# Optimization experiments

Measured on AMD Instinct MI355X. Metric: run time of the kernel, lower is better.

The kernel has to match this reference:

```python
import jax, jax.numpy as jnp
import numpy as np

INV_SQRT2 = np.float32(1.0 / np.sqrt(2.0))


def _dwt1(x, axis):
    # pywt db1 (Haar), even-length: cA=(even+odd)/sqrt2, cD=(even-odd)/sqrt2
    ev = jax.lax.slice_in_dim(x, 0, None, 2, axis)
    od = jax.lax.slice_in_dim(x, 1, None, 2, axis)
    return (ev + od) * INV_SQRT2, (ev - od) * INV_SQRT2


def _idwt1(lo, hi, axis):
    ev = (lo + hi) * INV_SQRT2
    od = (lo - hi) * INV_SQRT2
    st = jnp.stack([ev, od], axis=axis + 1)  # (.., n, 2, ..)
    new_shape = list(lo.shape)
    new_shape[axis] *= 2
    return st.reshape(new_shape)


def haar_dwt2(x):
    lo, hi = _dwt1(x, 1)      # along width
    ll, lh = _dwt1(lo, 0)     # along height
    hl, hh = _dwt1(hi, 0)
    return ll, lh, hl, hh


def haar_idwt2(ll, lh, hl, hh):
    lo = _idwt1(ll, lh, 0)
    hi = _idwt1(hl, hh, 0)
    return _idwt1(lo, hi, 1)


def conv_same(img, w, b):
    # img: [h, w] -> 1x1-channel SAME conv with bias
    y = jax.lax.conv_general_dilated(
        img[None, None], w, (1, 1), 'SAME',
        dimension_numbers=('NCHW', 'OIHW', 'NCHW'))
    return y[0, 0] + b[0]


def setup_inputs() -> dict:
    key = jax.random.key(0)
    ks = jax.random.split(key, 7)
    H = W = 4096
    return {
        'x': jax.random.normal(ks[0], (1, 1, H, W), dtype=jnp.float32),
        'w3': jax.random.normal(ks[1], (1, 1, 3, 3), dtype=jnp.float32) * 0.1,
        'b3': jax.random.normal(ks[2], (1,), dtype=jnp.float32) * 0.1,
        'w5': jax.random.normal(ks[3], (1, 1, 5, 5), dtype=jnp.float32) * 0.1,
        'b5': jax.random.normal(ks[4], (1,), dtype=jnp.float32) * 0.1,
        'w7': jax.random.normal(ks[5], (1, 1, 7, 7), dtype=jnp.float32) * 0.1,
        'b7': jax.random.normal(ks[6], (1,), dtype=jnp.float32) * 0.1,
    }


def reference(x, w3, b3, w5, b5, w7, b7):
    img = x[0, 0]
    # 3-level wavedec2: collect details finest -> coarsest
    details = []
    cur = img
    for _ in range(3):
        ll, lh, hl, hh = haar_dwt2(cur)
        details.append((lh, hl, hh))
        cur = ll
    # pywt coeff order is coarsest-first, so in the torch code:
    # HH1 = coarsest (3x3), HH2 = mid (5x5), HH3 = finest (7x7)
    lh_c, hl_c, hh_c = details[2]
    lh_m, hl_m, hh_m = details[1]
    lh_f, hl_f, hh_f = details[0]
    hh_c = conv_same(hh_c, w3, b3)
    hh_m = conv_same(hh_m, w5, b5)
    hh_f = conv_same(hh_f, w7, b7)
    # waverec2: coarsest -> finest
    rec = haar_idwt2(cur, lh_c, hl_c, hh_c)
    rec = haar_idwt2(rec, lh_m, hl_m, hh_m)
    rec = haar_idwt2(rec, lh_f, hl_f, hh_f)
    return rec[None, None]
```

## Files before the change

kernel.cpp:

```cpp
#include <hip/hip_runtime.h>
#include <stddef.h>

#define IMG_N 4096

typedef float vf4 __attribute__((ext_vector_type(4)));

#define S_LH1   0
#define S_HL1   1760
#define S_HH1   3520
#define S_LL1   5280
#define S_HH1C  7040
#define S_LL2   8192
#define S_LH2   8592
#define S_HL2   8992
#define S_HH2   9392
#define S_TOTAL 9792

#define S_HH2C  (S_HH1)
#define S_LL3   (S_HH1 + 320)
#define S_LH3   (S_HH1 + 420)
#define S_HL3   (S_HH1 + 520)
#define S_HH3   (S_HH1 + 620)
#define S_LL1P  (S_LL1)
#define S_LL2P  (S_LL1 + 1152)

__global__ __launch_bounds__(512, 8) void haar_fused(
    const float* __restrict__ x,
    const float* __restrict__ w3, const float* __restrict__ b3,
    const float* __restrict__ w5, const float* __restrict__ b5,
    const float* __restrict__ w7, const float* __restrict__ b7,
    float* __restrict__ out)
{
    __shared__ __align__(16) float sm[S_TOTAL];
    const int tid = threadIdx.x;
    const int bx = blockIdx.x, by = blockIdx.y;
    const int R0 = by * 64, C0 = bx * 64;

    float* LH1 = sm + S_LH1;   float* HL1 = sm + S_HL1;
    float* HH1 = sm + S_HH1;   float* LL1 = sm + S_LL1;
    float* HH1C = sm + S_HH1C;
    float* LL2 = sm + S_LL2;   float* LH2 = sm + S_LH2;
    float* HL2 = sm + S_HL2;   float* HH2 = sm + S_HH2;
    float* HH2C = sm + S_HH2C;
    float* LL3 = sm + S_LL3;   float* LH3 = sm + S_LH3;
    float* HL3 = sm + S_HL3;   float* HH3 = sm + S_HH3;
    float* LL1P = sm + S_LL1P; float* LL2P = sm + S_LL2P;

    const bool interior = (by >= 1) && (by <= 62) && (bx >= 1) && (bx <= 62);
    if (tid < 400) {
        const int u = tid / 10, g = tid % 10;
        float4 t0, t1, bb0, bb1;
        if (interior) {
            const float* p = x + (size_t)(R0 - 8 + 2 * u) * IMG_N + (C0 - 8 + 8 * g);
            t0  = *(const float4*)(p);
            t1  = *(const float4*)(p + 4);
            bb0 = *(const float4*)(p + IMG_N);
            bb1 = *(const float4*)(p + IMG_N + 4);
        } else {
            const int gr0 = R0 - 8 + 2 * u, gr1 = gr0 + 1;
            const int gc = C0 - 8 + 8 * g;
            const bool r0v = (gr0 >= 0 && gr0 < IMG_N), r1v = (gr1 >= 0 && gr1 < IMG_N);
            float tv[8], bv[8];
            #pragma unroll
            for (int k = 0; k < 8; ++k) {
                int gck = gc + k;
                bool cv = (gck >= 0 && gck < IMG_N);
                tv[k] = (r0v && cv) ? x[(size_t)gr0 * IMG_N + gck] : 0.0f;
                bv[k] = (r1v && cv) ? x[(size_t)gr1 * IMG_N + gck] : 0.0f;
            }
            t0  = make_float4(tv[0], tv[1], tv[2], tv[3]);
            t1  = make_float4(tv[4], tv[5], tv[6], tv[7]);
            bb0 = make_float4(bv[0], bv[1], bv[2], bv[3]);
            bb1 = make_float4(bv[4], bv[5], bv[6], bv[7]);
        }
        float4 llv, lhv, hlv, hhv;
        {
            float a = t0.x, b = t0.y, c = bb0.x, d = bb0.y;
            llv.x = (a + b + c + d) * 0.5f; lhv.x = (a + b - c - d) * 0.5f;
            hlv.x = (a - b + c - d) * 0.5f; hhv.x = (a - b - c + d) * 0.5f;
            a = t0.z; b = t0.w; c = bb0.z; d = bb0.w;
            llv.y = (a + b + c + d) * 0.5f; lhv.y = (a + b - c - d) * 0.5f;
            hlv.y = (a - b + c - d) * 0.5f; hhv.y = (a - b - c + d) * 0.5f;
            a = t1.x; b = t1.y; c = bb1.x; d = bb1.y;
            llv.z = (a + b + c + d) * 0.5f; lhv.z = (a + b - c - d) * 0.5f;
            hlv.z = (a - b + c - d) * 0.5f; hhv.z = (a - b - c + d) * 0.5f;
            a = t1.z; b = t1.w; c = bb1.z; d = bb1.w;
            llv.w = (a + b + c + d) * 0.5f; lhv.w = (a + b - c - d) * 0.5f;
            hlv.w = (a - b + c - d) * 0.5f; hhv.w = (a - b - c + d) * 0.5f;
        }
        const int o = u * 44 + 4 * g;
        *(float4*)(LL1 + o) = llv;  *(float4*)(LH1 + o) = lhv;
        *(float4*)(HL1 + o) = hlv;  *(float4*)(HH1 + o) = hhv;
    }
    __syncthreads();

    if (tid < 256) {
        const int i = tid >> 3;
        const int j0 = (tid & 7) << 2;
        const float bias = b7[0];
        float a0 = bias, a1 = bias, a2 = bias, a3 = bias;
        #pragma unroll
        for (int dy = 0; dy < 7; ++dy) {
            const float* rp = HH1 + (i + dy + 1) * 44 + j0;
            float4 A = *(const float4*)(rp);
            float4 B = *(const float4*)(rp + 4);
            float4 C = *(const float4*)(rp + 8);
            const float* wr = w7 + dy * 7;
            float q0 = wr[0], q1 = wr[1], q2 = wr[2], q3 = wr[3], q4 = wr[4],
                  q5 = wr[5], q6 = wr[6];
            a0 += q0*A.y + q1*A.z + q2*A.w + q3*B.x + q4*B.y + q5*B.z + q6*B.w;
            a1 += q0*A.z + q1*A.w + q2*B.x + q3*B.y + q4*B.z + q5*B.w + q6*C.x;
            a2 += q0*A.w + q1*B.x + q2*B.y + q3*B.z + q4*B.w + q5*C.x + q6*C.y;
            a3 += q0*B.x + q1*B.y + q2*B.z + q3*B.w + q4*C.x + q5*C.y + q6*C.z;
        }
        *(float4*)(HH1C + i * 36 + j0) = make_float4(a0, a1, a2, a3);
    } else if (tid < 356) {
        const int t = tid - 256;
        const int u = t / 5, g = t % 5;
        const float* rp = LL1 + (2 * u) * 44 + 8 * g;
        float4 t0 = *(const float4*)(rp),      t1 = *(const float4*)(rp + 4);
        float4 c0 = *(const float4*)(rp + 44), c1 = *(const float4*)(rp + 48);
        float4 llv, lhv, hlv, hhv;
        llv.x = (t0.x + t0.y + c0.x + c0.y) * 0.5f; lhv.x = (t0.x + t0.y - c0.x - c0.y) * 0.5f;
        hlv.x = (t0.x - t0.y + c0.x - c0.y) * 0.5f; hhv.x = (t0.x - t0.y - c0.x + c0.y) * 0.5f;
        llv.y = (t0.z + t0.w + c0.z + c0.w) * 0.5f; lhv.y = (t0.z + t0.w - c0.z - c0.w) * 0.5f;
        hlv.y = (t0.z - t0.w + c0.z - c0.w) * 0.5f; hhv.y = (t0.z - t0.w - c0.z + c0.w) * 0.5f;
        llv.z = (t1.x + t1.y + c1.x + c1.y) * 0.5f; lhv.z = (t1.x + t1.y - c1.x - c1.y) * 0.5f;
        hlv.z = (t1.x - t1.y + c1.x - c1.y) * 0.5f; hhv.z = (t1.x - t1.y - c1.x + c1.y) * 0.5f;
        llv.w = (t1.z + t1.w + c1.z + c1.w) * 0.5f; lhv.w = (t1.z + t1.w - c1.z - c1.w) * 0.5f;
        hlv.w = (t1.z - t1.w + c1.z - c1.w) * 0.5f; hhv.w = (t1.z - t1.w - c1.z + c1.w) * 0.5f;
        const int o = u * 20 + 4 * g;
        *(float4*)(LL2 + o) = llv;  *(float4*)(LH2 + o) = lhv;
        *(float4*)(HL2 + o) = hlv;  *(float4*)(HH2 + o) = hhv;
    }
    __syncthreads();

    if (tid < 50) {
        const int u = tid / 5, v2 = (tid % 5) * 2;
        const float* rp = LL2 + (2 * u) * 20 + 2 * v2;
        float4 t0 = *(const float4*)(rp);
        float4 c0 = *(const float4*)(rp + 20);
        const int o = u * 10 + v2;
        *(float2*)(LL3 + o) = make_float2((t0.x + t0.y + c0.x + c0.y) * 0.5f,
                                          (t0.z + t0.w + c0.z + c0.w) * 0.5f);
        *(float2*)(LH3 + o) = make_float2((t0.x + t0.y - c0.x - c0.y) * 0.5f,
                                          (t0.z + t0.w - c0.z - c0.w) * 0.5f);
        *(float2*)(HL3 + o) = make_float2((t0.x - t0.y + c0.x - c0.y) * 0.5f,
                                          (t0.z - t0.w + c0.z - c0.w) * 0.5f);
        *(float2*)(HH3 + o) = make_float2((t0.x - t0.y - c0.x + c0.y) * 0.5f,
                                          (t0.z - t0.w - c0.z + c0.w) * 0.5f);
    } else if (tid >= 64 && tid < 128) {
        const int s = tid - 64;
        const int i = s >> 2;
        const int j0 = (s & 3) << 2;
        const float bias = b5[0];
        float a0 = bias, a1 = bias, a2 = bias, a3 = bias;
        #pragma unroll
        for (int dy = 0; dy < 5; ++dy) {
            const float* rp = HH2 + (i + dy) * 20 + j0;
            float4 A = *(const float4*)(rp);
            float4 B = *(const float4*)(rp + 4);
            const float* wr = w5 + dy * 5;
            float q0 = wr[0], q1 = wr[1], q2 = wr[2], q3 = wr[3], q4 = wr[4];
            a0 += q0*A.x + q1*A.y + q2*A.z + q3*A.w + q4*B.x;
            a1 += q0*A.y + q1*A.z + q2*A.w + q3*B.x + q4*B.y;
            a2 += q0*A.z + q1*A.w + q2*B.x + q3*B.y + q4*B.z;
            a3 += q0*A.w + q1*B.x + q2*B.y + q3*B.z + q4*B.w;
        }
        *(float4*)(HH2C + i * 20 + j0) = make_float4(a0, a1, a2, a3);
    }
    __syncthreads();

    if (tid < 128) {
        const int p = tid >> 3, c = tid & 7;
        const int r = p >> 1;
        const float sr = (p & 1) ? -1.0f : 1.0f;
        float hh = b3[0];
        #pragma unroll
        for (int dy = 0; dy < 3; ++dy) {
            const float* row = HH3 + (r + dy) * 10 + c;
            const float* wr = w3 + dy * 3;
            hh += wr[0]*row[0] + wr[1]*row[1] + wr[2]*row[2];
        }
        const int li = (r + 1) * 10 + (c + 1);
        float lo = LL3[li] + sr * LH3[li];
        float hi = HL3[li] + sr * hh;
        *(float2*)(LL2P + p * 20 + 2 * c) =
            make_float2((lo + hi) * 0.5f, (lo - hi) * 0.5f);
    }
    __syncthreads();

    {
        const int p = tid >> 4, c = tid & 15;
        const int r = p >> 1;
        const float sr = (p & 1) ? -1.0f : 1.0f;
        const int li = (r + 2) * 20 + (c + 2);
        float lo = LL2P[r * 20 + c] + sr * LH2[li];
        float hi = HL2[li] + sr * HH2C[r * 20 + c];
        *(float2*)(LL1P + p * 36 + 2 * c) =
            make_float2((lo + hi) * 0.5f, (lo - hi) * 0.5f);
    }
    __syncthreads();

    #pragma unroll
    for (int k = 0; k < 2; ++k) {
        const int idx = tid + 512 * k;
        const int p = idx >> 4;
        const int c2 = (idx & 15) * 2;
        const int r = p >> 1;
        const float sr = (p & 1) ? -1.0f : 1.0f;
        const int li = (r + 4) * 44 + (c2 + 4);
        const int ci = r * 36 + c2;
        float2 llp = *(const float2*)(LL1P + ci);
        float2 lh  = *(const float2*)(LH1 + li);
        float2 hl  = *(const float2*)(HL1 + li);
        float2 hhc = *(const float2*)(HH1C + ci);
        float lo0 = llp.x + sr * lh.x;
        float hi0 = hl.x + sr * hhc.x;
        float lo1 = llp.y + sr * lh.y;
        float hi1 = hl.y + sr * hhc.y;
        vf4 o = { (lo0 + hi0) * 0.5f, (lo0 - hi0) * 0.5f,
                  (lo1 + hi1) * 0.5f, (lo1 - hi1) * 0.5f };
        __builtin_nontemporal_store(
            o, (vf4*)(out + (size_t)(R0 + p) * IMG_N + C0 + 2 * c2));
    }
}

extern "C" void kernel_launch(void* const* d_in, const int* in_sizes, int n_in,
                              void* d_out, int out_size, void* d_ws, size_t ws_size,
                              hipStream_t stream) {
    (void)in_sizes; (void)n_in; (void)out_size; (void)d_ws; (void)ws_size;
    const float* x  = (const float*)d_in[0];
    const float* w3 = (const float*)d_in[1];
    const float* b3 = (const float*)d_in[2];
    const float* w5 = (const float*)d_in[3];
    const float* b5 = (const float*)d_in[4];
    const float* w7 = (const float*)d_in[5];
    const float* b7 = (const float*)d_in[6];
    float* out = (float*)d_out;

    dim3 grid(IMG_N / 64, IMG_N / 64);
    dim3 block(512);
    haar_fused<<<grid, block, 0, stream>>>(x, w3, b3, w5, b5, w7, b7, out);
}
```

Before: 133.4 us.

## Run coarse wavelet levels in one wavefront with wave fences, not block barriers

The level-2 and level-3 decomposition, the 5x5 conv and the coarsest reconstruction now all run inside a single 64-lane wavefront. That wavefront uses wave-level fences instead of block-wide __syncthreads, which removes two block barriers. Meanwhile 128 threads each compute two output rows of the 7x7 conv and share the row loads between them. The shared-memory row stride drops from 44 to 40 and the scratch regions are laid out again without aliasing, which enlarges total LDS a little. In exchange, the critical path becomes serial work on one wave, and the conv threads carry more registers.

```diff
diff --git a/kernel.cpp b/kernel.cpp
--- a/kernel.cpp
+++ b/kernel.cpp
@@ -6,23 +6,29 @@
 typedef float vf4 __attribute__((ext_vector_type(4)));
 
 #define S_LH1   0
-#define S_HL1   1760
-#define S_HH1   3520
-#define S_LL1   5280
-#define S_HH1C  7040
-#define S_LL2   8192
-#define S_LH2   8592
-#define S_HL2   8992
-#define S_HH2   9392
-#define S_TOTAL 9792
-
-#define S_HH2C  (S_HH1)
-#define S_LL3   (S_HH1 + 320)
-#define S_LH3   (S_HH1 + 420)
-#define S_HL3   (S_HH1 + 520)
-#define S_HH3   (S_HH1 + 620)
+#define S_HL1   1600
+#define S_HH1   3200
+#define S_LL1   4800
+#define S_HH1C  6400
+#define S_LL2   7552
+#define S_LH2   7952
+#define S_HL2   8352
+#define S_HH2   8752
+#define S_HH2C  9152
+#define S_LL3   9472
+#define S_LH3   9572
+#define S_HL3   9672
+#define S_HH3   9772
+#define S_LL2P  9872
+#define S_TOTAL 10192
+
 #define S_LL1P  (S_LL1)
-#define S_LL2P  (S_LL1 + 1152)
+
+static __device__ __forceinline__ void wave_fence() {
+    __builtin_amdgcn_wave_barrier();
+    __builtin_amdgcn_s_waitcnt(0);
+    __builtin_amdgcn_wave_barrier();
+}
 
 __global__ __launch_bounds__(512, 8) void haar_fused(
     const float* __restrict__ x,
@@ -88,105 +94,127 @@
             llv.w = (a + b + c + d) * 0.5f; lhv.w = (a + b - c - d) * 0.5f;
             hlv.w = (a - b + c - d) * 0.5f; hhv.w = (a - b - c + d) * 0.5f;
         }
-        const int o = u * 44 + 4 * g;
+        const int o = u * 40 + 4 * g;
         *(float4*)(LL1 + o) = llv;  *(float4*)(LH1 + o) = lhv;
         *(float4*)(HL1 + o) = hlv;  *(float4*)(HH1 + o) = hhv;
     }
     __syncthreads();
 
-    if (tid < 256) {
-        const int i = tid >> 3;
+    if (tid < 128) {
+        const int i2 = tid >> 3;
         const int j0 = (tid & 7) << 2;
         const float bias = b7[0];
         float a0 = bias, a1 = bias, a2 = bias, a3 = bias;
+        float c0 = bias, c1 = bias, c2 = bias, c3 = bias;
         #pragma unroll
-        for (int dy = 0; dy < 7; ++dy) {
-            const float* rp = HH1 + (i + dy + 1) * 44 + j0;
+        for (int k = 0; k < 8; ++k) {
+            const float* rp = HH1 + (2 * i2 + 1 + k) * 40 + j0;
             float4 A = *(const float4*)(rp);
             float4 B = *(const float4*)(rp + 4);
             float4 C = *(const float4*)(rp + 8);
-            const float* wr = w7 + dy * 7;
-            float q0 = wr[0], q1 = wr[1], q2 = wr[2], q3 = wr[3], q4 = wr[4],
-                  q5 = wr[5], q6 = wr[6];
-            a0 += q0*A.y + q1*A.z + q2*A.w + q3*B.x + q4*B.y + q5*B.z + q6*B.w;
-            a1 += q0*A.z + q1*A.w + q2*B.x + q3*B.y + q4*B.z + q5*B.w + q6*C.x;
-            a2 += q0*A.w + q1*B.x + q2*B.y + q3*B.z + q4*B.w + q5*C.x + q6*C.y;
-            a3 += q0*B.x + q1*B.y + q2*B.z + q3*B.w + q4*C.x + q5*C.y + q6*C.z;
-        }
-        *(float4*)(HH1C + i * 36 + j0) = make_float4(a0, a1, a2, a3);
-    } else if (tid < 356) {
-        const int t = tid - 256;
-        const int u = t / 5, g = t % 5;
-        const float* rp = LL1 + (2 * u) * 44 + 8 * g;
-        float4 t0 = *(const float4*)(rp),      t1 = *(const float4*)(rp + 4);
-        float4 c0 = *(const float4*)(rp + 44), c1 = *(const float4*)(rp + 48);
-        float4 llv, lhv, hlv, hhv;
-        llv.x = (t0.x + t0.y + c0.x + c0.y) * 0.5f; lhv.x = (t0.x + t0.y - c0.x - c0.y) * 0.5f;
-        hlv.x = (t0.x - t0.y + c0.x - c0.y) * 0.5f; hhv.x = (t0.x - t0.y - c0.x + c0.y) * 0.5f;
-        llv.y = (t0.z + t0.w + c0.z + c0.w) * 0.5f; lhv.y = (t0.z + t0.w - c0.z - c0.w) * 0.5f;
-        hlv.y = (t0.z - t0.w + c0.z - c0.w) * 0.5f; hhv.y = (t0.z - t0.w - c0.z + c0.w) * 0.5f;
-        llv.z = (t1.x + t1.y + c1.x + c1.y) * 0.5f; lhv.z = (t1.x + t1.y - c1.x - c1.y) * 0.5f;
-        hlv.z = (t1.x - t1.y + c1.x - c1.y) * 0.5f; hhv.z = (t1.x - t1.y - c1.x + c1.y) * 0.5f;
-        llv.w = (t1.z + t1.w + c1.z + c1.w) * 0.5f; lhv.w = (t1.z + t1.w - c1.z - c1.w) * 0.5f;
-        hlv.w = (t1.z - t1.w + c1.z - c1.w) * 0.5f; hhv.w = (t1.z - t1.w - c1.z + c1.w) * 0.5f;
-        const int o = u * 20 + 4 * g;
-        *(float4*)(LL2 + o) = llv;  *(float4*)(LH2 + o) = lhv;
-        *(float4*)(HL2 + o) = hlv;  *(float4*)(HH2 + o) = hhv;
-    }
-    __syncthreads();
-
-    if (tid < 50) {
-        const int u = tid / 5, v2 = (tid % 5) * 2;
-        const float* rp = LL2 + (2 * u) * 20 + 2 * v2;
-        float4 t0 = *(const float4*)(rp);
-        float4 c0 = *(const float4*)(rp + 20);
-        const int o = u * 10 + v2;
-        *(float2*)(LL3 + o) = make_float2((t0.x + t0.y + c0.x + c0.y) * 0.5f,
-                                          (t0.z + t0.w + c0.z + c0.w) * 0.5f);
-        *(float2*)(LH3 + o) = make_float2((t0.x + t0.y - c0.x - c0.y) * 0.5f,
-                                          (t0.z + t0.w - c0.z - c0.w) * 0.5f);
-        *(float2*)(HL3 + o) = make_float2((t0.x - t0.y + c0.x - c0.y) * 0.5f,
-                                          (t0.z - t0.w + c0.z - c0.w) * 0.5f);
-        *(float2*)(HH3 + o) = make_float2((t0.x - t0.y - c0.x + c0.y) * 0.5f,
-                                          (t0.z - t0.w - c0.z + c0.w) * 0.5f);
-    } else if (tid >= 64 && tid < 128) {
-        const int s = tid - 64;
-        const int i = s >> 2;
-        const int j0 = (s & 3) << 2;
-        const float bias = b5[0];
-        float a0 = bias, a1 = bias, a2 = bias, a3 = bias;
+            if (k <= 6) {
+                const float* wr = w7 + k * 7;
+                float q0 = wr[0], q1 = wr[1], q2 = wr[2], q3 = wr[3],
+                      q4 = wr[4], q5 = wr[5], q6 = wr[6];
+                a0 += q0*A.y + q1*A.z + q2*A.w + q3*B.x + q4*B.y + q5*B.z + q6*B.w;
+                a1 += q0*A.z + q1*A.w + q2*B.x + q3*B.y + q4*B.z + q5*B.w + q6*C.x;
+                a2 += q0*A.w + q1*B.x + q2*B.y + q3*B.z + q4*B.w + q5*C.x + q6*C.y;
+                a3 += q0*B.x + q1*B.y + q2*B.z + q3*B.w + q4*C.x + q5*C.y + q6*C.z;
+            }
+            if (k >= 1) {
+                const float* wr = w7 + (k - 1) * 7;
+                float q0 = wr[0], q1 = wr[1], q2 = wr[2], q3 = wr[3],
+                      q4 = wr[4], q5 = wr[5], q6 = wr[6];
+                c0 += q0*A.y + q1*A.z + q2*A.w + q3*B.x + q4*B.y + q5*B.z + q6*B.w;
+                c1 += q0*A.z + q1*A.w + q2*B.x + q3*B.y + q4*B.z + q5*B.w + q6*C.x;
+                c2 += q0*A.w + q1*B.x + q2*B.y + q3*B.z + q4*B.w + q5*C.x + q6*C.y;
+                c3 += q0*B.x + q1*B.y + q2*B.z + q3*B.w + q4*C.x + q5*C.y + q6*C.z;
+            }
+        }
+        *(float4*)(HH1C + (2 * i2) * 36 + j0)     = make_float4(a0, a1, a2, a3);
+        *(float4*)(HH1C + (2 * i2 + 1) * 36 + j0) = make_float4(c0, c1, c2, c3);
+    } else if (tid >= 256 && tid < 320) {
+        const int lane = tid - 256;
         #pragma unroll
-        for (int dy = 0; dy < 5; ++dy) {
-            const float* rp = HH2 + (i + dy) * 20 + j0;
-            float4 A = *(const float4*)(rp);
-            float4 B = *(const float4*)(rp + 4);
-            const float* wr = w5 + dy * 5;
-            float q0 = wr[0], q1 = wr[1], q2 = wr[2], q3 = wr[3], q4 = wr[4];
-            a0 += q0*A.x + q1*A.y + q2*A.z + q3*A.w + q4*B.x;
-            a1 += q0*A.y + q1*A.z + q2*A.w + q3*B.x + q4*B.y;
-            a2 += q0*A.z + q1*A.w + q2*B.x + q3*B.y + q4*B.z;
-            a3 += q0*A.w + q1*B.x + q2*B.y + q3*B.z + q4*B.w;
-        }
-        *(float4*)(HH2C + i * 20 + j0) = make_float4(a0, a1, a2, a3);
-    }
-    __syncthreads();
-
-    if (tid < 128) {
-        const int p = tid >> 3, c = tid & 7;
-        const int r = p >> 1;
-        const float sr = (p & 1) ? -1.0f : 1.0f;
-        float hh = b3[0];
-        #pragma unroll
-        for (int dy = 0; dy < 3; ++dy) {
-            const float* row = HH3 + (r + dy) * 10 + c;
-            const float* wr = w3 + dy * 3;
-            hh += wr[0]*row[0] + wr[1]*row[1] + wr[2]*row[2];
-        }
-        const int li = (r + 1) * 10 + (c + 1);
-        float lo = LL3[li] + sr * LH3[li];
-        float hi = HL3[li] + sr * hh;
-        *(float2*)(LL2P + p * 20 + 2 * c) =
-            make_float2((lo + hi) * 0.5f, (lo - hi) * 0.5f);
+        for (int k = 0; k < 2; ++k) {
+            const int t = lane + 64 * k;
+            if (t < 100) {
+                const int u = t / 5, g = t % 5;
+                const float* rp = LL1 + (2 * u) * 40 + 8 * g;
+                float4 t0 = *(const float4*)(rp),      t1 = *(const float4*)(rp + 4);
+                float4 c0 = *(const float4*)(rp + 40), c1 = *(const float4*)(rp + 44);
+                float4 llv, lhv, hlv, hhv;
+                llv.x = (t0.x + t0.y + c0.x + c0.y) * 0.5f; lhv.x = (t0.x + t0.y - c0.x - c0.y) * 0.5f;
+                hlv.x = (t0.x - t0.y + c0.x - c0.y) * 0.5f; hhv.x = (t0.x - t0.y - c0.x + c0.y) * 0.5f;
+                llv.y = (t0.z + t0.w + c0.z + c0.w) * 0.5f; lhv.y = (t0.z + t0.w - c0.z - c0.w) * 0.5f;
+                hlv.y = (t0.z - t0.w + c0.z - c0.w) * 0.5f; hhv.y = (t0.z - t0.w - c0.z + c0.w) * 0.5f;
+                llv.z = (t1.x + t1.y + c1.x + c1.y) * 0.5f; lhv.z = (t1.x + t1.y - c1.x - c1.y) * 0.5f;
+                hlv.z = (t1.x - t1.y + c1.x - c1.y) * 0.5f; hhv.z = (t1.x - t1.y - c1.x + c1.y) * 0.5f;
+                llv.w = (t1.z + t1.w + c1.z + c1.w) * 0.5f; lhv.w = (t1.z + t1.w - c1.z - c1.w) * 0.5f;
+                hlv.w = (t1.z - t1.w + c1.z - c1.w) * 0.5f; hhv.w = (t1.z - t1.w - c1.z + c1.w) * 0.5f;
+                const int o = u * 20 + 4 * g;
+                *(float4*)(LL2 + o) = llv;  *(float4*)(LH2 + o) = lhv;
+                *(float4*)(HL2 + o) = hlv;  *(float4*)(HH2 + o) = hhv;
+            }
+        }
+        wave_fence();
+        if (lane < 50) {
+            const int u = lane / 5, v2 = (lane % 5) * 2;
+            const float* rp = LL2 + (2 * u) * 20 + 2 * v2;
+            float4 t0 = *(const float4*)(rp);
+            float4 c0 = *(const float4*)(rp + 20);
+            const int o = u * 10 + v2;
+            *(float2*)(LL3 + o) = make_float2((t0.x + t0.y + c0.x + c0.y) * 0.5f,
+                                              (t0.z + t0.w + c0.z + c0.w) * 0.5f);
+            *(float2*)(LH3 + o) = make_float2((t0.x + t0.y - c0.x - c0.y) * 0.5f,
+                                              (t0.z + t0.w - c0.z - c0.w) * 0.5f);
+            *(float2*)(HL3 + o) = make_float2((t0.x - t0.y + c0.x - c0.y) * 0.5f,
+                                              (t0.z - t0.w + c0.z - c0.w) * 0.5f);
+            *(float2*)(HH3 + o) = make_float2((t0.x - t0.y - c0.x + c0.y) * 0.5f,
+                                              (t0.z - t0.w - c0.z + c0.w) * 0.5f);
+        }
+        {
+            const int i = lane >> 2;
+            const int j0 = (lane & 3) << 2;
+            const float bias = b5[0];
+            float a0 = bias, a1 = bias, a2 = bias, a3 = bias;
+            #pragma unroll
+            for (int dy = 0; dy < 5; ++dy) {
+                const float* rp = HH2 + (i + dy) * 20 + j0;
+                float4 A = *(const float4*)(rp);
+                float4 B = *(const float4*)(rp + 4);
+                const float* wr = w5 + dy * 5;
+                float q0 = wr[0], q1 = wr[1], q2 = wr[2], q3 = wr[3], q4 = wr[4];
+                a0 += q0*A.x + q1*A.y + q2*A.z + q3*A.w + q4*B.x;
+                a1 += q0*A.y + q1*A.z + q2*A.w + q3*B.x + q4*B.y;
+                a2 += q0*A.z + q1*A.w + q2*B.x + q3*B.y + q4*B.z;
+                a3 += q0*A.w + q1*B.x + q2*B.y + q3*B.z + q4*B.w;
+            }
+            *(float4*)(HH2C + i * 20 + j0) = make_float4(a0, a1, a2, a3);
+        }
+        wave_fence();
+        {
+            const float b3c = b3[0];
+            #pragma unroll
+            for (int k = 0; k < 2; ++k) {
+                const int item = lane + 64 * k;
+                const int p = item >> 3, c = item & 7;
+                const int r = p >> 1;
+                const float sr = (p & 1) ? -1.0f : 1.0f;
+                float hh = b3c;
+                #pragma unroll
+                for (int dy = 0; dy < 3; ++dy) {
+                    const float* row = HH3 + (r + dy) * 10 + c;
+                    const float* wr = w3 + dy * 3;
+                    hh += wr[0]*row[0] + wr[1]*row[1] + wr[2]*row[2];
+                }
+                const int li = (r + 1) * 10 + (c + 1);
+                float lo = LL3[li] + sr * LH3[li];
+                float hi = HL3[li] + sr * hh;
+                *(float2*)(LL2P + p * 20 + 2 * c) =
+                    make_float2((lo + hi) * 0.5f, (lo - hi) * 0.5f);
+            }
+        }
     }
     __syncthreads();
 
@@ -209,7 +237,7 @@
         const int c2 = (idx & 15) * 2;
         const int r = p >> 1;
         const float sr = (p & 1) ? -1.0f : 1.0f;
-        const int li = (r + 4) * 44 + (c2 + 4);
+        const int li = (r + 4) * 40 + (c2 + 4);
         const int ci = r * 36 + c2;
         float2 llp = *(const float2*)(LL1P + ci);
         float2 lh  = *(const float2*)(LH1 + li);
```

New measurement: 200.6 us. +50.4%, slower.
